# Optimization experiments

Measured on AMD Instinct MI355X. Metric: run time of the kernel, lower is better.

## Reference

```python
import jax, jax.numpy as jnp
from jax import lax
import numpy as np

K = 3  # kernel size per dim, dimension=6 -> 3**6 = 729 taps
OFFS = np.stack(np.meshgrid(*([np.arange(K)] * 6), indexing='ij'), axis=-1).reshape(-1, 6).astype(np.int32)


def conv6d(x, kernel):
    """Dense emulation of a 1->1 channel MinkowskiConvolution over 6 spatial dims.

    x: (b, s, s, d, d, d, d) with zeros at absent sparse coordinates.
    kernel: (729,) flattened 3^6 kernel (in=out=1 channel, no bias).
    Zeros at absent coordinates contribute nothing to the gathered sums, so the
    dense conv equals the sparse conv evaluated everywhere.
    """
    xp = jnp.pad(x, [(0, 0)] + [(1, 1)] * 6)
    offs = jnp.asarray(OFFS)
    zero = jnp.int32(0)

    def body(acc, ow):
        off, wt = ow
        sl = lax.dynamic_slice(
            xp, (zero, off[0], off[1], off[2], off[3], off[4], off[5]), x.shape)
        return acc + wt * sl, None

    acc, _ = lax.scan(jax.checkpoint(body), jnp.zeros_like(x), (offs, kernel))
    return acc


def _transpose6d(t):
    # swap the two scale dims and the two image-coordinate pairs:
    # (b, s1, s2, h1, w1, h2, w2) -> (b, s2, s1, h2, w2, h1, w1)
    return jnp.transpose(t, (0, 2, 1, 5, 6, 3, 4))


def setup_inputs() -> dict:
    key = jax.random.key(0)
    k1, k2 = jax.random.split(key)
    x = jax.random.normal(k1, (1, 2, 2, 32, 32, 32, 32), dtype=jnp.float32)
    kernel = jax.random.normal(k2, (K ** 6,), dtype=jnp.float32) * 0.05
    return {"x": x, "kernel": kernel}


def reference(x, kernel):
    # MinkowskiConvolution outputs at the input coordinate set; MinkowskiSigmoid
    # acts on features at those coordinates; to_dense() zero-fills elsewhere.
    # Dense equivalent: mask to the input nonzero set.
    mask = (x != 0).astype(x.dtype)
    branch = lambda z: jax.nn.sigmoid(conv6d(jax.nn.relu(z), kernel))
    # symmetric mode: conv(x) + T(conv(T(x))); T(coords(T(x))) == coords(x)
    y = mask * (branch(x) + _transpose6d(branch(_transpose6d(x))))
    b, s1, s2, d1, d2, d3, d4 = y.shape
    y = y.reshape(b, s1 * s2, d1, d2, d3, d4).sum(axis=1)  # (b, h1, w1, h2, w2)
    return y
```

## Files before the change

kernel.cpp:

```cpp
#include <hip/hip_runtime.h>

typedef _Float16 half8 __attribute__((ext_vector_type(8)));
typedef float f16v __attribute__((ext_vector_type(16)));
typedef float f4 __attribute__((ext_vector_type(4)));
typedef unsigned long long ull;

#define X_SLAB   1048576
#define PLANE_BYTES (34*36*4*2)
#define RPT_SITES (34*34*34*36)
#define RPT_OFF  65536
#define RPT_SLACK 4096
#define TAB_N    (3*6*3*512)
#define TAB_ELEMS  (4*81*8)

__global__ __launch_bounds__(256)
void prep(const float* __restrict__ x, const float* __restrict__ w,
          ull* __restrict__ rpt, _Float16* __restrict__ tabm) {
    unsigned s = blockIdx.x * 256 + threadIdx.x;
    if (s < RPT_SITES) {
        unsigned q = s;
        int j4 = q % 36; q /= 36;
        int j3 = q % 34; q /= 34;
        int j2 = q % 34; q /= 34;
        int j1 = q;
        union { _Float16 h[4]; ull u; } pk;
        pk.u = 0ull;
        if (j1 >= 1 && j1 <= 32 && j2 >= 1 && j2 <= 32 &&
            j3 >= 1 && j3 <= 32 && j4 >= 1 && j4 <= 32) {
            size_t off = (size_t)(j1-1)*32768 + (j2-1)*1024 + (j3-1)*32 + (j4-1);
            #pragma unroll
            for (int t = 0; t < 4; ++t)
                pk.h[t] = (_Float16)fmaxf(x[(size_t)t*X_SLAB + off], 0.f);
        }
        rpt[s] = pk.u;
    }
    if (blockIdx.x == 0) {
        for (int idx = threadIdx.x; idx < TAB_N; idx += 256) {
            int j = idx & 7, l = (idx >> 3) & 63, slice = idx >> 9;
            int p4 = slice % 3, j2rel = (slice/3) % 6, p2 = slice/18;
            int n32 = l & 31;
            int d2 = n32 >> 3, n8 = n32 & 7;
            int k = 8*(l>>5) + j;
            int p5h = k >> 2, t = k & 3;
            int p3 = j2rel - d2;
            float val = 0.f;
            if (p5h < 3 && p3 >= 0 && p3 <= 2) {
                int br = n8 & 1, sc = n8 >> 1, s1 = sc >> 1, s2 = sc & 1;
                int t1 = t >> 1, t2 = t & 1;
                int a = t1 - s1 + 1, b = t2 - s2 + 1;
                int widx = (br == 0)
                    ? (a*243 + b*81 + p2*27 + p3*9 + p4*3 + p5h)
                    : (b*243 + a*81 + p4*27 + p5h*9 + p2*3 + p3);
                val = w[widx];
            }
            tabm[idx] = (_Float16)val;
        }
    }
}

__global__ __launch_bounds__(256)
void conv_mfma(const float* __restrict__ x, const ull* __restrict__ rpt,
               const _Float16* __restrict__ tabm, float* __restrict__ out) {
    __shared__ __align__(16) unsigned char arena[2*12288 + 4096];
    unsigned char* msk = arena + 24576;

    const int tid  = threadIdx.x;
    const int lane = tid & 63;
    const int wv   = tid >> 6;
    const int e2b  = blockIdx.x * 4;
    const int e1   = blockIdx.y;
    const size_t blockbase = (size_t)e1*32768 + (size_t)e2b*1024;

    {
        int p0 = tid * 16;
        #pragma unroll
        for (int g = 0; g < 4; ++g) {
            f4 a0 = *(const f4*)(x + (size_t)0*X_SLAB + blockbase + p0 + 4*g);
            f4 a1 = *(const f4*)(x + (size_t)1*X_SLAB + blockbase + p0 + 4*g);
            f4 a2 = *(const f4*)(x + (size_t)2*X_SLAB + blockbase + p0 + 4*g);
            f4 a3 = *(const f4*)(x + (size_t)3*X_SLAB + blockbase + p0 + 4*g);
            unsigned wbits = 0;
            #pragma unroll
            for (int q = 0; q < 4; ++q) {
                unsigned b = (a0[q] != 0.f ? 1u : 0u) | (a1[q] != 0.f ? 2u : 0u)
                           | (a2[q] != 0.f ? 4u : 0u) | (a3[q] != 0.f ? 8u : 0u);
                wbits |= b << (8*q);
            }
            *(unsigned*)&msk[p0 + 4*g] = wbits;
        }
    }

    f16v acc[8];
    #pragma unroll
    for (int r = 0; r < 8; ++r)
        #pragma unroll
        for (int i = 0; i < 16; ++i) acc[r][i] = 0.f;

    const int R   = wv * 8;
    const int j4b = (lane & 31) + 2*(lane >> 5);

    half8 Bn[3];
    {
        const char* pgb = (const char*)rpt + ((size_t)(e1+0)*34 + (e2b+0))*PLANE_BYTES;
        #pragma unroll
        for (int kk = 0; kk < 3; ++kk) {
            int off = (tid + kk*256) * 16;
            __builtin_amdgcn_global_load_lds(
                (const __attribute__((address_space(1))) unsigned int*)(pgb + off),
                (__attribute__((address_space(3))) unsigned int*)(arena + off),
                16, 0, 0);
        }
        const _Float16* tb = tabm + lane*8;
        Bn[0] = *(const half8*)(tb);
        Bn[1] = *(const half8*)(tb + 512);
        Bn[2] = *(const half8*)(tb + 1024);
    }

    #pragma unroll 1
    for (int it = 0; it < 18; ++it) {
        const int buf = it & 1;
        __syncthreads();
        half8 B0 = Bn[0], B1 = Bn[1], B2 = Bn[2];
        if (it + 1 < 18) {
            const int nit = it + 1;
            const int p2 = nit / 6, j2 = nit % 6;
            const char* pgb = (const char*)rpt
                            + ((size_t)(e1+p2)*34 + (e2b+j2)) * PLANE_BYTES;
            char* dst = (char*)arena + (buf^1)*12288;
            #pragma unroll
            for (int kk = 0; kk < 3; ++kk) {
                int off = (tid + kk*256) * 16;
                __builtin_amdgcn_global_load_lds(
                    (const __attribute__((address_space(1))) unsigned int*)(pgb + off),
                    (__attribute__((address_space(3))) unsigned int*)(dst + off),
                    16, 0, 0);
            }
            const _Float16* tb = tabm + (size_t)nit*1536 + lane*8;
            Bn[0] = *(const half8*)(tb);
            Bn[1] = *(const half8*)(tb + 512);
            Bn[2] = *(const half8*)(tb + 1024);
        }
        const _Float16* planeh = (const _Float16*)(arena + buf*12288);
        #pragma unroll
        for (int j3l = 0; j3l < 10; ++j3l) {
            const ull* ap = (const ull*)(planeh + ((R + j3l)*36 + j4b)*4);
            union { ull u[2]; half8 h; } A;
            A.u[0] = ap[0]; A.u[1] = ap[1];
            if (j3l <= 7)
                acc[j3l]   = __builtin_amdgcn_mfma_f32_32x32x16_f16(A.h, B0, acc[j3l],   0,0,0);
            if (j3l >= 1 && j3l <= 8)
                acc[j3l-1] = __builtin_amdgcn_mfma_f32_32x32x16_f16(A.h, B1, acc[j3l-1], 0,0,0);
            if (j3l >= 2)
                acc[j3l-2] = __builtin_amdgcn_mfma_f32_32x32x16_f16(A.h, B2, acc[j3l-2], 0,0,0);
        }
    }

    const int n8 = lane & 7;
    const int d2 = (lane >> 3) & 3;
    const int h  = lane >> 5;
    const int sbit = n8 >> 1;
    float* outp = out + blockbase + (size_t)d2*1024;
    #pragma unroll
    for (int rloc = 0; rloc < 8; ++rloc) {
        const int e3 = R + rloc;
        float v[16];
        #pragma unroll
        for (int g = 0; g < 4; ++g) {
            unsigned mw = *(const unsigned*)&msk[d2*1024 + e3*32 + 8*g + 4*h];
            #pragma unroll
            for (int j = 0; j < 4; ++j) {
                float a  = acc[rloc][4*g + j];
                float sg = __builtin_amdgcn_rcpf(1.f + __expf(-a));
                v[4*g+j] = ((mw >> (8*j + sbit)) & 1u) ? sg : 0.f;
            }
        }
        #pragma unroll
        for (int i = 0; i < 16; ++i) {
            v[i] += __shfl_xor(v[i], 1);
            v[i] += __shfl_xor(v[i], 2);
            v[i] += __shfl_xor(v[i], 4);
        }
        if (n8 == 0) {
            #pragma unroll
            for (int g = 0; g < 4; ++g) {
                f4 o; o.x = v[4*g]; o.y = v[4*g+1]; o.z = v[4*g+2]; o.w = v[4*g+3];
                *(f4*)(outp + e3*32 + 8*g + 4*h) = o;
            }
        }
    }
}

__global__ void build_wtab(const float* __restrict__ w, float* __restrict__ tab) {
    int idx = blockIdx.x * blockDim.x + threadIdx.x;
    if (idx >= TAB_ELEMS) return;
    int n  = idx & 7;
    int r  = idx >> 3;
    int p5 = r % 3; r /= 3;
    int p4 = r % 3; r /= 3;
    int p3 = r % 3; r /= 3;
    int p2 = r % 3; r /= 3;
    int t  = r;
    int t1 = t >> 1, t2 = t & 1;
    int br = n & 1;
    int s  = n >> 1;
    int s1 = s >> 1, s2 = s & 1;
    int a = t1 - s1 + 1;
    int b = t2 - s2 + 1;
    int widx = (br == 0)
        ? (a*243 + b*81 + p2*27 + p3*9 + p4*3 + p5)
        : (b*243 + a*81 + p4*27 + p5*9 + p2*3 + p3);
    tab[idx] = w[widx];
}

__global__ __launch_bounds__(256)
void conv_fp32(const float* __restrict__ x,
               const float* __restrict__ tab,
               float* __restrict__ out) {
    const int e4 = threadIdx.x;
    const int e3 = blockIdx.x * 8 + threadIdx.y;
    const int e2 = blockIdx.y;
    const int e1 = blockIdx.z;

    float acc[8];
    #pragma unroll
    for (int n = 0; n < 8; ++n) acc[n] = 0.f;

    #pragma unroll 1
    for (int t = 0; t < 4; ++t) {
        const float* st  = x + (size_t)t * X_SLAB;
        const float* wt0 = tab + t * 648;
        #pragma unroll
        for (int p2 = 0; p2 < 3; ++p2) {
            #pragma unroll
            for (int p3 = 0; p3 < 3; ++p3) {
                int i1 = e1 + p2 - 1, i2 = e2 + p3 - 1;
                bool v12 = ((unsigned)i1 < 32u) && ((unsigned)i2 < 32u);
                const float* base = st + (i1*32768 + i2*1024 + (e3-1)*32 + (e4-1));
                const float* wt = wt0 + (p2*3 + p3) * 72;
                #pragma unroll
                for (int p4 = 0; p4 < 3; ++p4) {
                    int i3 = e3 + p4 - 1;
                    bool v3 = v12 && ((unsigned)i3 < 32u);
                    #pragma unroll
                    for (int p5 = 0; p5 < 3; ++p5) {
                        int i4 = e4 + p5 - 1;
                        bool ok = v3 && ((unsigned)i4 < 32u);
                        float v = ok ? fmaxf(base[p4*32 + p5], 0.f) : 0.f;
                        const float* w8 = wt + (p4*3 + p5)*8;
                        #pragma unroll
                        for (int n = 0; n < 8; ++n)
                            acc[n] = fmaf(w8[n], v, acc[n]);
                    }
                }
            }
        }
    }

    const size_t eflat = (size_t)e1*32768 + e2*1024 + e3*32 + e4;
    float res = 0.f;
    #pragma unroll
    for (int i = 0; i < 4; ++i) {
        float xv = x[(size_t)i * X_SLAB + eflat];
        float s0 = __builtin_amdgcn_rcpf(1.f + __expf(-acc[2*i]));
        float s1 = __builtin_amdgcn_rcpf(1.f + __expf(-acc[2*i+1]));
        float m  = (xv != 0.f) ? 1.f : 0.f;
        res = fmaf(m, s0 + s1, res);
    }
    out[eflat] = res;
}

extern "C" void kernel_launch(void* const* d_in, const int* in_sizes, int n_in,
                              void* d_out, int out_size, void* d_ws, size_t ws_size,
                              hipStream_t stream) {
    const float* x = (const float*)d_in[0];
    const float* w = (const float*)d_in[1];
    float* out = (float*)d_out;

    const size_t need = (size_t)RPT_OFF + (size_t)RPT_SITES*8ull + RPT_SLACK;

    if (ws_size >= need) {
        _Float16* tabm = (_Float16*)d_ws;
        ull*      rpt  = (ull*)((char*)d_ws + RPT_OFF);
        prep<<<dim3((RPT_SITES + 255)/256), dim3(256), 0, stream>>>(x, w, rpt, tabm);
        dim3 grd(8, 32, 1), blk(256, 1, 1);
        conv_mfma<<<grd, blk, 0, stream>>>(x, rpt, tabm, out);
    } else {
        float* tab = (float*)d_ws;
        build_wtab<<<dim3((TAB_ELEMS + 255)/256), dim3(256), 0, stream>>>(w, tab);
        dim3 blk(32, 8, 1), grd(4, 32, 32);
        conv_fp32<<<grd, blk, 0, stream>>>(x, tab, out);
    }
}
```

Measured before the change: 104.2 us.

## Split conv blocks along e3 and read A operands directly from global memory

The grid doubles by splitting each block's e3 rows in half along a new z dimension, so each wave now holds 4 accumulators instead of 8. The double-buffered LDS staging of rpt planes through global_load_lds, along with its per-iteration barriers, is removed. Each wave now loads its A fragments straight from global memory and relies on cache for reuse. This gives more blocks and lower register pressure for better occupancy, at the cost of redundant global/L2 traffic for overlapping rows and no explicit prefetch overlap.

```diff
diff --git a/kernel.cpp b/kernel.cpp
--- a/kernel.cpp
+++ b/kernel.cpp
@@ -61,24 +61,26 @@
 __global__ __launch_bounds__(256)
 void conv_mfma(const float* __restrict__ x, const ull* __restrict__ rpt,
                const _Float16* __restrict__ tabm, float* __restrict__ out) {
-    __shared__ __align__(16) unsigned char arena[2*12288 + 4096];
-    unsigned char* msk = arena + 24576;
+    __shared__ unsigned char msk[2048];
 
     const int tid  = threadIdx.x;
     const int lane = tid & 63;
     const int wv   = tid >> 6;
     const int e2b  = blockIdx.x * 4;
     const int e1   = blockIdx.y;
-    const size_t blockbase = (size_t)e1*32768 + (size_t)e2b*1024;
+    const int bz   = blockIdx.z;
+    const size_t pbase = (size_t)e1*32768 + (size_t)e2b*1024 + (size_t)bz*512;
 
     {
-        int p0 = tid * 16;
-        #pragma unroll
-        for (int g = 0; g < 4; ++g) {
-            f4 a0 = *(const f4*)(x + (size_t)0*X_SLAB + blockbase + p0 + 4*g);
-            f4 a1 = *(const f4*)(x + (size_t)1*X_SLAB + blockbase + p0 + 4*g);
-            f4 a2 = *(const f4*)(x + (size_t)2*X_SLAB + blockbase + p0 + 4*g);
-            f4 a3 = *(const f4*)(x + (size_t)3*X_SLAB + blockbase + p0 + 4*g);
+        int p0 = tid * 8;
+        int d2 = p0 >> 9, rem = p0 & 511;
+        const float* xb = x + pbase + (size_t)d2*1024 + rem;
+        #pragma unroll
+        for (int g = 0; g < 2; ++g) {
+            f4 a0 = *(const f4*)(xb + (size_t)0*X_SLAB + 4*g);
+            f4 a1 = *(const f4*)(xb + (size_t)1*X_SLAB + 4*g);
+            f4 a2 = *(const f4*)(xb + (size_t)2*X_SLAB + 4*g);
+            f4 a3 = *(const f4*)(xb + (size_t)3*X_SLAB + 4*g);
             unsigned wbits = 0;
             #pragma unroll
             for (int q = 0; q < 4; ++q) {
@@ -89,69 +91,44 @@
             *(unsigned*)&msk[p0 + 4*g] = wbits;
         }
     }
-
-    f16v acc[8];
-    #pragma unroll
-    for (int r = 0; r < 8; ++r)
+    __syncthreads();
+
+    f16v acc[4];
+    #pragma unroll
+    for (int r = 0; r < 4; ++r)
         #pragma unroll
         for (int i = 0; i < 16; ++i) acc[r][i] = 0.f;
 
-    const int R   = wv * 8;
+    const int R   = bz*16 + wv*4;
     const int j4b = (lane & 31) + 2*(lane >> 5);
-
-    half8 Bn[3];
-    {
-        const char* pgb = (const char*)rpt + ((size_t)(e1+0)*34 + (e2b+0))*PLANE_BYTES;
-        #pragma unroll
-        for (int kk = 0; kk < 3; ++kk) {
-            int off = (tid + kk*256) * 16;
-            __builtin_amdgcn_global_load_lds(
-                (const __attribute__((address_space(1))) unsigned int*)(pgb + off),
-                (__attribute__((address_space(3))) unsigned int*)(arena + off),
-                16, 0, 0);
-        }
-        const _Float16* tb = tabm + lane*8;
-        Bn[0] = *(const half8*)(tb);
-        Bn[1] = *(const half8*)(tb + 512);
-        Bn[2] = *(const half8*)(tb + 1024);
-    }
+    const char* awave = (const char*)rpt + (size_t)(R*36 + j4b)*8;
 
     #pragma unroll 1
-    for (int it = 0; it < 18; ++it) {
-        const int buf = it & 1;
-        __syncthreads();
-        half8 B0 = Bn[0], B1 = Bn[1], B2 = Bn[2];
-        if (it + 1 < 18) {
-            const int nit = it + 1;
-            const int p2 = nit / 6, j2 = nit % 6;
-            const char* pgb = (const char*)rpt
-                            + ((size_t)(e1+p2)*34 + (e2b+j2)) * PLANE_BYTES;
-            char* dst = (char*)arena + (buf^1)*12288;
-            #pragma unroll
-            for (int kk = 0; kk < 3; ++kk) {
-                int off = (tid + kk*256) * 16;
-                __builtin_amdgcn_global_load_lds(
-                    (const __attribute__((address_space(1))) unsigned int*)(pgb + off),
-                    (__attribute__((address_space(3))) unsigned int*)(dst + off),
-                    16, 0, 0);
-            }
-            const _Float16* tb = tabm + (size_t)nit*1536 + lane*8;
-            Bn[0] = *(const half8*)(tb);
-            Bn[1] = *(const half8*)(tb + 512);
-            Bn[2] = *(const half8*)(tb + 1024);
-        }
-        const _Float16* planeh = (const _Float16*)(arena + buf*12288);
-        #pragma unroll
-        for (int j3l = 0; j3l < 10; ++j3l) {
-            const ull* ap = (const ull*)(planeh + ((R + j3l)*36 + j4b)*4);
-            union { ull u[2]; half8 h; } A;
-            A.u[0] = ap[0]; A.u[1] = ap[1];
-            if (j3l <= 7)
-                acc[j3l]   = __builtin_amdgcn_mfma_f32_32x32x16_f16(A.h, B0, acc[j3l],   0,0,0);
-            if (j3l >= 1 && j3l <= 8)
-                acc[j3l-1] = __builtin_amdgcn_mfma_f32_32x32x16_f16(A.h, B1, acc[j3l-1], 0,0,0);
-            if (j3l >= 2)
-                acc[j3l-2] = __builtin_amdgcn_mfma_f32_32x32x16_f16(A.h, B2, acc[j3l-2], 0,0,0);
+    for (int p2 = 0; p2 < 3; ++p2) {
+        #pragma unroll 2
+        for (int j2 = 0; j2 < 6; ++j2) {
+            const int it = p2*6 + j2;
+            const char* aptr = awave + ((size_t)(e1+p2)*34 + (e2b+j2))*PLANE_BYTES;
+            const _Float16* tb = tabm + it*1536 + lane*8;
+            half8 B0 = *(const half8*)(tb);
+            half8 B1 = *(const half8*)(tb + 512);
+            half8 B2 = *(const half8*)(tb + 1024);
+            union { ull u[2]; half8 h; } A[6];
+            #pragma unroll
+            for (int j3l = 0; j3l < 6; ++j3l) {
+                const ull* ap = (const ull*)(aptr + j3l*288);
+                A[j3l].u[0] = ap[0];
+                A[j3l].u[1] = ap[1];
+            }
+            #pragma unroll
+            for (int j3l = 0; j3l < 6; ++j3l) {
+                if (j3l <= 3)
+                    acc[j3l]   = __builtin_amdgcn_mfma_f32_32x32x16_f16(A[j3l].h, B0, acc[j3l],   0,0,0);
+                if (j3l >= 1 && j3l <= 4)
+                    acc[j3l-1] = __builtin_amdgcn_mfma_f32_32x32x16_f16(A[j3l].h, B1, acc[j3l-1], 0,0,0);
+                if (j3l >= 2)
+                    acc[j3l-2] = __builtin_amdgcn_mfma_f32_32x32x16_f16(A[j3l].h, B2, acc[j3l-2], 0,0,0);
+            }
         }
     }
 
@@ -159,14 +136,14 @@
     const int d2 = (lane >> 3) & 3;
     const int h  = lane >> 5;
     const int sbit = n8 >> 1;
-    float* outp = out + blockbase + (size_t)d2*1024;
-    #pragma unroll
-    for (int rloc = 0; rloc < 8; ++rloc) {
-        const int e3 = R + rloc;
+    float* outp = out + pbase + (size_t)d2*1024;
+    #pragma unroll
+    for (int rloc = 0; rloc < 4; ++rloc) {
+        const int e3loc = wv*4 + rloc;
         float v[16];
         #pragma unroll
         for (int g = 0; g < 4; ++g) {
-            unsigned mw = *(const unsigned*)&msk[d2*1024 + e3*32 + 8*g + 4*h];
+            unsigned mw = *(const unsigned*)&msk[d2*512 + e3loc*32 + 8*g + 4*h];
             #pragma unroll
             for (int j = 0; j < 4; ++j) {
                 float a  = acc[rloc][4*g + j];
@@ -184,7 +161,7 @@
             #pragma unroll
             for (int g = 0; g < 4; ++g) {
                 f4 o; o.x = v[4*g]; o.y = v[4*g+1]; o.z = v[4*g+2]; o.w = v[4*g+3];
-                *(f4*)(outp + e3*32 + 8*g + 4*h) = o;
+                *(f4*)(outp + e3loc*32 + 8*g + 4*h) = o;
             }
         }
     }
@@ -282,7 +259,7 @@
         _Float16* tabm = (_Float16*)d_ws;
         ull*      rpt  = (ull*)((char*)d_ws + RPT_OFF);
         prep<<<dim3((RPT_SITES + 255)/256), dim3(256), 0, stream>>>(x, w, rpt, tabm);
-        dim3 grd(8, 32, 1), blk(256, 1, 1);
+        dim3 grd(8, 32, 2), blk(256, 1, 1);
         conv_mfma<<<grd, blk, 0, stream>>>(x, rpt, tabm, out);
     } else {
         float* tab = (float*)d_ws;
```

New measurement: 104.8 us. No clear change (+0.6%).
